# Kernel tuning notes

Hardware: AMD Instinct MI355X
Metric: run time of the kernel (lower is better)

Reference implementation:

```python
import jax, jax.numpy as jnp
import numpy as np

NODE_DIM = 128
NUM_IRREPS = 224          # 128 + 64 + 32 gates (one per irrep channel)
SPH_DIM = 480             # 128*1 + 64*3 + 32*5
HIDDEN = NODE_DIM + 2 * NUM_IRREPS  # 576
NUM_BASIS = 20
N_NODES = 10000
N_EDGES = 160000
# Each gate scalar is broadcast over its irrep's (2l+1) components.
_REPEATS = np.array([1] * 128 + [3] * 64 + [5] * 32)


def _expand_gate(g):
    # [E, 224] -> [E, 480], repeating each gate over its irrep dimension
    return jnp.repeat(g, _REPEATS, axis=-1, total_repeat_length=SPH_DIM)


def setup_inputs() -> dict:
    key = jax.random.key(0)
    ks = jax.random.split(key, 12)
    x_scalar = jax.random.normal(ks[0], (N_NODES, NODE_DIM), dtype=jnp.float32)
    x_spherical = jax.random.normal(ks[1], (N_NODES, SPH_DIM), dtype=jnp.float32)
    rbf = jax.random.uniform(ks[2], (N_EDGES, NUM_BASIS), dtype=jnp.float32)
    fcut = jax.random.uniform(ks[3], (N_EDGES, 1), dtype=jnp.float32)
    rsh = jax.random.normal(ks[4], (N_EDGES, SPH_DIM), dtype=jnp.float32)
    edge_index = jax.random.randint(ks[5], (2, N_EDGES), 0, N_NODES, dtype=jnp.int64)
    s1 = 1.0 / np.sqrt(NODE_DIM)
    s2 = 1.0 / np.sqrt(NUM_BASIS)
    W1 = jax.random.uniform(ks[6], (NODE_DIM, NODE_DIM), jnp.float32, -s1, s1)
    b1 = jnp.zeros((NODE_DIM,), jnp.float32)
    W2 = jax.random.uniform(ks[7], (NODE_DIM, HIDDEN), jnp.float32, -s1, s1)
    b2 = jnp.zeros((HIDDEN,), jnp.float32)
    Wr = jax.random.uniform(ks[8], (NUM_BASIS, HIDDEN), jnp.float32, -s2, s2)
    br = jnp.zeros((HIDDEN,), jnp.float32)
    return {"x_scalar": x_scalar, "x_spherical": x_spherical, "rbf": rbf,
            "fcut": fcut, "rsh": rsh, "edge_index": edge_index,
            "W1": W1, "b1": b1, "W2": W2, "b2": b2, "Wr": Wr, "br": br}


def reference(x_scalar, x_spherical, rbf, fcut, rsh, edge_index,
              W1, b1, W2, b2, Wr, br):
    src, dst = edge_index[0], edge_index[1]
    # scalar MLP: Linear -> SiLU -> Linear
    scalar_out = jax.nn.silu(x_scalar @ W1 + b1) @ W2 + b2          # [N, 576]
    filter_weight = (rbf @ Wr + br) * fcut                          # [E, 576]
    filter_out = scalar_out[dst] * filter_weight                    # [E, 576]
    gate_state = filter_out[:, :NUM_IRREPS]                         # [E, 224]
    gate_edge = filter_out[:, NUM_IRREPS:2 * NUM_IRREPS]            # [E, 224]
    message_scalar = filter_out[:, 2 * NUM_IRREPS:]                 # [E, 128]
    # ElementwiseTensorProduct(edge_irreps, '224x0e'): per-channel scalar gating
    message_spherical = (x_spherical[dst] * _expand_gate(gate_state)
                         + rsh * _expand_gate(gate_edge))           # [E, 480]
    new_scalar = x_scalar.at[src].add(message_scalar)
    new_spherical = x_spherical.at[src].add(message_spherical)
    return (new_scalar, new_spherical)
```

## Files before the change

kernel.cpp:

```cpp
#include <hip/hip_runtime.h>

#define NODE_DIM 128
#define NUM_IRREPS 224
#define SPH_DIM 480
#define HIDDEN 576
#define NUM_BASIS 20
#define N_NODES 10000
#define N_EDGES 160000
#define NPB 8

__global__ void init_out(const float* __restrict__ xs,
                         const float* __restrict__ xsp,
                         float* __restrict__ out,
                         int* __restrict__ counts) {
    const int stride = gridDim.x * blockDim.x;
    const int t0 = blockIdx.x * blockDim.x + threadIdx.x;
    for (int i = t0; i < N_NODES * NODE_DIM; i += stride) out[i] = xs[i];
    float* o2 = out + (size_t)N_NODES * NODE_DIM;
    for (int i = t0; i < N_NODES * SPH_DIM; i += stride) o2[i] = xsp[i];
    for (int i = t0; i < N_NODES; i += stride) counts[i] = 0;
}

__global__ __launch_bounds__(128) void node_mlp(
    const float* __restrict__ x,
    const float* __restrict__ W1, const float* __restrict__ b1,
    const float* __restrict__ W2, const float* __restrict__ b2,
    float* __restrict__ so) {
    __shared__ float xs[NPB][NODE_DIM];
    __shared__ float hs[NPB][NODE_DIM];
    const int tid = threadIdx.x;
    const int n0 = blockIdx.x * NPB;

    #pragma unroll
    for (int n = 0; n < NPB; ++n) {
        int node = n0 + n;
        xs[n][tid] = (node < N_NODES) ? x[(size_t)node * NODE_DIM + tid] : 0.f;
    }
    __syncthreads();

    float acc[NPB];
    #pragma unroll
    for (int n = 0; n < NPB; ++n) acc[n] = b1[tid];
    for (int k = 0; k < NODE_DIM; ++k) {
        float w = W1[k * NODE_DIM + tid];
        #pragma unroll
        for (int n = 0; n < NPB; ++n) acc[n] = fmaf(xs[n][k], w, acc[n]);
    }
    #pragma unroll
    for (int n = 0; n < NPB; ++n) {
        float v = acc[n];
        hs[n][tid] = v / (1.f + __expf(-v));
    }
    __syncthreads();

    for (int j = tid; j < HIDDEN; j += 128) {
        float a2[NPB];
        #pragma unroll
        for (int n = 0; n < NPB; ++n) a2[n] = b2[j];
        for (int k = 0; k < NODE_DIM; ++k) {
            float w = W2[k * HIDDEN + j];
            #pragma unroll
            for (int n = 0; n < NPB; ++n) a2[n] = fmaf(hs[n][k], w, a2[n]);
        }
        #pragma unroll
        for (int n = 0; n < NPB; ++n) {
            int node = n0 + n;
            if (node < N_NODES) so[(size_t)node * HIDDEN + j] = a2[n];
        }
    }
}

__global__ __launch_bounds__(256) void hist_kernel(const int* __restrict__ eidx,
                                                   int* __restrict__ counts) {
    int i = blockIdx.x * blockDim.x + threadIdx.x;
    if (i < N_EDGES) atomicAdd(&counts[eidx[i]], 1);
}

__global__ __launch_bounds__(1024) void scan_kernel(const int* __restrict__ counts,
                                                    int* __restrict__ offsets,
                                                    int* __restrict__ cursor) {
    __shared__ int wsum[16];
    const int tid = threadIdx.x;
    int vals[10];
    int run = 0;
    #pragma unroll
    for (int i = 0; i < 10; ++i) {
        int idx = tid * 10 + i;
        int c = (idx < N_NODES) ? counts[idx] : 0;
        vals[i] = run;
        run += c;
    }
    const int lane = tid & 63, w = tid >> 6;
    int inc = run;
    #pragma unroll
    for (int off = 1; off < 64; off <<= 1) {
        int v = __shfl_up(inc, off);
        if (lane >= off) inc += v;
    }
    if (lane == 63) wsum[w] = inc;
    __syncthreads();
    if (w == 0) {
        int v = (lane < 16) ? wsum[lane] : 0;
        #pragma unroll
        for (int off = 1; off < 16; off <<= 1) {
            int u = __shfl_up(v, off);
            if (lane >= off) v += u;
        }
        if (lane < 16) wsum[lane] = v;
    }
    __syncthreads();
    const int wbase = (w > 0) ? wsum[w - 1] : 0;
    const int base = wbase + inc - run;
    #pragma unroll
    for (int i = 0; i < 10; ++i) {
        int idx = tid * 10 + i;
        if (idx < N_NODES) {
            int v = base + vals[i];
            offsets[idx] = v;
            cursor[idx] = v;
        }
    }
    if (tid == 1023) offsets[N_NODES] = wbase + inc;
}

__global__ __launch_bounds__(256) void scatter_kernel(const int* __restrict__ eidx,
                                                      int* __restrict__ cursor,
                                                      int* __restrict__ edge_order) {
    int i = blockIdx.x * blockDim.x + threadIdx.x;
    if (i < N_EDGES) {
        int s = eidx[i];
        int pos = atomicAdd(&cursor[s], 1);
        edge_order[pos] = i;
    }
}

#define DOT20(a, WREG) do { \
    a = fmaf(q0.x, WREG[0], a);  a = fmaf(q0.y, WREG[1], a);  a = fmaf(q0.z, WREG[2], a);  a = fmaf(q0.w, WREG[3], a); \
    a = fmaf(q1.x, WREG[4], a);  a = fmaf(q1.y, WREG[5], a);  a = fmaf(q1.z, WREG[6], a);  a = fmaf(q1.w, WREG[7], a); \
    a = fmaf(q2.x, WREG[8], a);  a = fmaf(q2.y, WREG[9], a);  a = fmaf(q2.z, WREG[10], a); a = fmaf(q2.w, WREG[11], a); \
    a = fmaf(q3.x, WREG[12], a); a = fmaf(q3.y, WREG[13], a); a = fmaf(q3.z, WREG[14], a); a = fmaf(q3.w, WREG[15], a); \
    a = fmaf(q4.x, WREG[16], a); a = fmaf(q4.y, WREG[17], a); a = fmaf(q4.z, WREG[18], a); a = fmaf(q4.w, WREG[19], a); \
} while (0)

#define LOAD_PAYLOAD() do { \
    const float4* rq = (const float4*)(rbf + (size_t)eC * NUM_BASIS); \
    q0 = rq[0]; q1 = rq[1]; q2 = rq[2]; q3 = rq[3]; q4 = rq[4]; \
    const float* sod = so + (size_t)dC * HIDDEN; \
    s0 = sod[j0]; s1 = sod[j1]; \
    if (has2) s2 = sod[j2]; \
    const float* xd = xsp + (size_t)dC * SPH_DIM + d0; \
    const float* rd = rsh + (size_t)eC * SPH_DIM + d0; \
    x0 = xd[0]; r0 = rd[0]; \
    if (nd > 1) { x1 = xd[1]; r1 = rd[1]; } \
    if (nd > 2) { x2 = xd[2]; r2 = rd[2]; } \
} while (0)

__global__ __launch_bounds__(256, 4) void node_gather(
    const float* __restrict__ xsp,
    const float* __restrict__ rbf, const float* __restrict__ fcut,
    const float* __restrict__ rsh, const int* __restrict__ eidx,
    const float* __restrict__ Wr, const float* __restrict__ br,
    const float* __restrict__ so,
    const int* __restrict__ offsets, const int* __restrict__ edge_order,
    float* __restrict__ out_scalar, float* __restrict__ out_sph)
{
    const int t = threadIdx.x;
    const int n = blockIdx.x;
    const bool dup  = (t >= 224);
    const int  r    = dup ? (t - 32) : t;
    const int  j0   = r;
    const int  j1   = NUM_IRREPS + r;
    const bool has2 = (t < 128);
    const int  j2   = 2 * NUM_IRREPS + (t & 127);

    int nd, d0;
    if (t < 128)      { nd = 1; d0 = t; }
    else if (t < 192) { nd = 3; d0 = 128 + (t - 128) * 3; }
    else if (t < 224) { nd = 3; d0 = 320 + (t - 192) * 5; }
    else              { nd = 2; d0 = 320 + (t - 224) * 5 + 3; }

    float wr0[NUM_BASIS], wr1[NUM_BASIS], wr2[NUM_BASIS];
    #pragma unroll
    for (int k = 0; k < NUM_BASIS; ++k) {
        wr0[k] = Wr[k * HIDDEN + j0];
        wr1[k] = Wr[k * HIDDEN + j1];
        wr2[k] = has2 ? Wr[k * HIDDEN + j2] : 0.f;
    }
    const float br0 = br[j0], br1 = br[j1], br2 = has2 ? br[j2] : 0.f;

    const int beg  = offsets[n];
    const int end_ = offsets[n + 1];

    float accS = 0.f, accD0 = 0.f, accD1 = 0.f, accD2 = 0.f;

    if (beg < end_) {
        const int last = end_ - 1;
        const int i1 = min(beg + 1, last);
        const int i2 = min(beg + 2, last);
        const int i3 = min(beg + 3, last);
        int   eC = edge_order[beg];
        int   e1 = edge_order[i1];
        int   e2 = edge_order[i2];
        int   e3 = edge_order[i3];
        int   dC = eidx[N_EDGES + eC]; float fC = fcut[eC];
        int   d1 = eidx[N_EDGES + e1]; float f1 = fcut[e1];
        int   d2 = eidx[N_EDGES + e2]; float f2 = fcut[e2];

        float4 q0, q1, q2, q3, q4;
        float  s0, s1, s2 = 0.f, x0, x1 = 0.f, x2 = 0.f, r0, r1 = 0.f, r2 = 0.f;
        LOAD_PAYLOAD();

        for (int idx = beg; idx <= last; ++idx) {
            float a0 = br0, a1 = br1, a2 = br2;
            DOT20(a0, wr0);
            DOT20(a1, wr1);
            if (has2) { DOT20(a2, wr2); }
            const float fo0 = a0 * fC * s0;
            const float fo1 = a1 * fC * s1;
            if (has2) accS = fmaf(a2 * fC, s2, accS);
            accD0 = fmaf(x0, fo0, fmaf(r0, fo1, accD0));
            if (nd > 1) accD1 = fmaf(x1, fo0, fmaf(r1, fo1, accD1));
            if (nd > 2) accD2 = fmaf(x2, fo0, fmaf(r2, fo1, accD2));

            eC = e1; dC = d1; fC = f1;
            e1 = e2; d1 = d2; f1 = f2;
            LOAD_PAYLOAD();
            e2 = e3;
            d2 = eidx[N_EDGES + e3]; f2 = fcut[e3];
            e3 = edge_order[min(idx + 4, last)];
        }
    }

    if (t < 128) out_scalar[(size_t)n * NODE_DIM + t] += accS;
    float* od = out_sph + (size_t)n * SPH_DIM + d0;
    od[0] += accD0;
    if (nd > 1) od[1] += accD1;
    if (nd > 2) od[2] += accD2;
}

extern "C" void kernel_launch(void* const* d_in, const int* in_sizes, int n_in,
                              void* d_out, int out_size, void* d_ws, size_t ws_size,
                              hipStream_t stream) {
    const float* x_scalar    = (const float*)d_in[0];
    const float* x_spherical = (const float*)d_in[1];
    const float* rbf         = (const float*)d_in[2];
    const float* fcut        = (const float*)d_in[3];
    const float* rsh         = (const float*)d_in[4];
    const int*   eidx        = (const int*)d_in[5];
    const float* W1          = (const float*)d_in[6];
    const float* b1          = (const float*)d_in[7];
    const float* W2          = (const float*)d_in[8];
    const float* b2          = (const float*)d_in[9];
    const float* Wr          = (const float*)d_in[10];
    const float* br          = (const float*)d_in[11];

    float* out        = (float*)d_out;
    float* out_scalar = out;
    float* out_sph    = out + (size_t)N_NODES * NODE_DIM;

    float* scalar_out = (float*)d_ws;
    int*   counts     = (int*)(scalar_out + (size_t)N_NODES * HIDDEN);
    int*   offsets    = counts + N_NODES;
    int*   cursor     = offsets + N_NODES + 1;
    int*   edge_order = cursor + N_NODES;

    init_out<<<2048, 256, 0, stream>>>(x_scalar, x_spherical, out, counts);
    hist_kernel<<<(N_EDGES + 255) / 256, 256, 0, stream>>>(eidx, counts);
    scan_kernel<<<1, 1024, 0, stream>>>(counts, offsets, cursor);
    scatter_kernel<<<(N_EDGES + 255) / 256, 256, 0, stream>>>(eidx, cursor, edge_order);
    node_mlp<<<(N_NODES + NPB - 1) / NPB, 128, 0, stream>>>(x_scalar, W1, b1, W2, b2, scalar_out);
    node_gather<<<N_NODES, 256, 0, stream>>>(x_spherical, rbf, fcut, rsh, eidx,
                                             Wr, br, scalar_out, offsets, edge_order,
                                             out_scalar, out_sph);
}
```

Before: 335.5 us.

## Rebalance gather threads to 320 and double-buffer edge payload loads

The node gather kernel now uses 320 threads per block. The first 256 threads handle the spherical output and 64 extra threads each handle two scalar message channels, so no thread computes a third 20-wide dot product. The edge loop is unrolled by two with ping-pong payload registers, index prefetch runs deeper, and empty asm statements pin the Wr weights in VGPRs. The node MLP nodes-per-block also drops from 8 to 4. In exchange, per-thread register use goes up and each block carries an extra wavefront.

```diff
diff --git a/kernel.cpp b/kernel.cpp
--- a/kernel.cpp
+++ b/kernel.cpp
@@ -7,7 +7,7 @@
 #define NUM_BASIS 20
 #define N_NODES 10000
 #define N_EDGES 160000
-#define NPB 8
+#define NPB 4
 
 __global__ void init_out(const float* __restrict__ xs,
                          const float* __restrict__ xsp,
@@ -134,28 +134,51 @@
     }
 }
 
-#define DOT20(a, WREG) do { \
-    a = fmaf(q0.x, WREG[0], a);  a = fmaf(q0.y, WREG[1], a);  a = fmaf(q0.z, WREG[2], a);  a = fmaf(q0.w, WREG[3], a); \
-    a = fmaf(q1.x, WREG[4], a);  a = fmaf(q1.y, WREG[5], a);  a = fmaf(q1.z, WREG[6], a);  a = fmaf(q1.w, WREG[7], a); \
-    a = fmaf(q2.x, WREG[8], a);  a = fmaf(q2.y, WREG[9], a);  a = fmaf(q2.z, WREG[10], a); a = fmaf(q2.w, WREG[11], a); \
-    a = fmaf(q3.x, WREG[12], a); a = fmaf(q3.y, WREG[13], a); a = fmaf(q3.z, WREG[14], a); a = fmaf(q3.w, WREG[15], a); \
-    a = fmaf(q4.x, WREG[16], a); a = fmaf(q4.y, WREG[17], a); a = fmaf(q4.z, WREG[18], a); a = fmaf(q4.w, WREG[19], a); \
+#define PIN20(W) asm volatile("" : \
+ "+v"(W[0]),"+v"(W[1]),"+v"(W[2]),"+v"(W[3]),"+v"(W[4]), \
+ "+v"(W[5]),"+v"(W[6]),"+v"(W[7]),"+v"(W[8]),"+v"(W[9]), \
+ "+v"(W[10]),"+v"(W[11]),"+v"(W[12]),"+v"(W[13]),"+v"(W[14]), \
+ "+v"(W[15]),"+v"(W[16]),"+v"(W[17]),"+v"(W[18]),"+v"(W[19]))
+
+#define DOT20(a, W, Q0,Q1,Q2,Q3,Q4) do { \
+    a = fmaf(Q0.x, W[0], a);  a = fmaf(Q0.y, W[1], a);  a = fmaf(Q0.z, W[2], a);  a = fmaf(Q0.w, W[3], a); \
+    a = fmaf(Q1.x, W[4], a);  a = fmaf(Q1.y, W[5], a);  a = fmaf(Q1.z, W[6], a);  a = fmaf(Q1.w, W[7], a); \
+    a = fmaf(Q2.x, W[8], a);  a = fmaf(Q2.y, W[9], a);  a = fmaf(Q2.z, W[10], a); a = fmaf(Q2.w, W[11], a); \
+    a = fmaf(Q3.x, W[12], a); a = fmaf(Q3.y, W[13], a); a = fmaf(Q3.z, W[14], a); a = fmaf(Q3.w, W[15], a); \
+    a = fmaf(Q4.x, W[16], a); a = fmaf(Q4.y, W[17], a); a = fmaf(Q4.z, W[18], a); a = fmaf(Q4.w, W[19], a); \
 } while (0)
 
-#define LOAD_PAYLOAD() do { \
-    const float4* rq = (const float4*)(rbf + (size_t)eC * NUM_BASIS); \
-    q0 = rq[0]; q1 = rq[1]; q2 = rq[2]; q3 = rq[3]; q4 = rq[4]; \
-    const float* sod = so + (size_t)dC * HIDDEN; \
-    s0 = sod[j0]; s1 = sod[j1]; \
-    if (has2) s2 = sod[j2]; \
-    const float* xd = xsp + (size_t)dC * SPH_DIM + d0; \
-    const float* rd = rsh + (size_t)eC * SPH_DIM + d0; \
-    x0 = xd[0]; r0 = rd[0]; \
-    if (nd > 1) { x1 = xd[1]; r1 = rd[1]; } \
-    if (nd > 2) { x2 = xd[2]; r2 = rd[2]; } \
+#define LOADP(Q0,Q1,Q2,Q3,Q4, S0,S1, X0,X1,X2, R0,R1,R2, E, D) do { \
+    const float4* rq = (const float4*)(rbf + (size_t)(E) * NUM_BASIS); \
+    Q0 = rq[0]; Q1 = rq[1]; Q2 = rq[2]; Q3 = rq[3]; Q4 = rq[4]; \
+    const float* sod = so + (size_t)(D) * HIDDEN; \
+    S0 = sod[c0]; S1 = sod[c1]; \
+    if (sphMode) { \
+        const float* xd = xsp + (size_t)(D) * SPH_DIM + db; \
+        const float* rd = rsh + (size_t)(E) * SPH_DIM + db; \
+        X0 = xd[0]; R0 = rd[0]; \
+        if (nd > 1) { X1 = xd[1]; R1 = rd[1]; } \
+        if (nd > 2) { X2 = xd[2]; R2 = rd[2]; } \
+    } \
 } while (0)
 
-__global__ __launch_bounds__(256, 4) void node_gather(
+#define COMPUTE(Q0,Q1,Q2,Q3,Q4, S0,S1, X0,X1,X2, R0,R1,R2, FC) do { \
+    float a0 = bc0, a1 = bc1; \
+    DOT20(a0, w0, Q0,Q1,Q2,Q3,Q4); \
+    DOT20(a1, w1, Q0,Q1,Q2,Q3,Q4); \
+    if (sphMode) { \
+        const float fo0 = a0 * (FC) * S0; \
+        const float fo1 = a1 * (FC) * S1; \
+        accD0 = fmaf(X0, fo0, fmaf(R0, fo1, accD0)); \
+        if (nd > 1) accD1 = fmaf(X1, fo0, fmaf(R1, fo1, accD1)); \
+        if (nd > 2) accD2 = fmaf(X2, fo0, fmaf(R2, fo1, accD2)); \
+    } else { \
+        accA = fmaf(a0 * (FC), S0, accA); \
+        accB = fmaf(a1 * (FC), S1, accB); \
+    } \
+} while (0)
+
+__global__ __launch_bounds__(320, 3) void node_gather(
     const float* __restrict__ xsp,
     const float* __restrict__ rbf, const float* __restrict__ fcut,
     const float* __restrict__ rsh, const int* __restrict__ eidx,
@@ -166,76 +189,80 @@
 {
     const int t = threadIdx.x;
     const int n = blockIdx.x;
-    const bool dup  = (t >= 224);
-    const int  r    = dup ? (t - 32) : t;
-    const int  j0   = r;
-    const int  j1   = NUM_IRREPS + r;
-    const bool has2 = (t < 128);
-    const int  j2   = 2 * NUM_IRREPS + (t & 127);
-
-    int nd, d0;
-    if (t < 128)      { nd = 1; d0 = t; }
-    else if (t < 192) { nd = 3; d0 = 128 + (t - 128) * 3; }
-    else if (t < 224) { nd = 3; d0 = 320 + (t - 192) * 5; }
-    else              { nd = 2; d0 = 320 + (t - 224) * 5 + 3; }
-
-    float wr0[NUM_BASIS], wr1[NUM_BASIS], wr2[NUM_BASIS];
+    const bool sphMode = (t < 256);
+
+    int c0, c1;
+    if (t < 224)      { c0 = t;                  c1 = NUM_IRREPS + t; }
+    else if (t < 256) { c0 = t - 32;             c1 = NUM_IRREPS + (t - 32); }
+    else              { c0 = 448 + 2 * (t - 256); c1 = c0 + 1; }
+
+    int nd, db;
+    if (t < 128)      { nd = 1; db = t; }
+    else if (t < 192) { nd = 3; db = 128 + (t - 128) * 3; }
+    else if (t < 224) { nd = 3; db = 320 + (t - 192) * 5; }
+    else if (t < 256) { nd = 2; db = 320 + (t - 224) * 5 + 3; }
+    else              { nd = 0; db = 0; }
+
+    float w0[NUM_BASIS], w1[NUM_BASIS];
     #pragma unroll
     for (int k = 0; k < NUM_BASIS; ++k) {
-        wr0[k] = Wr[k * HIDDEN + j0];
-        wr1[k] = Wr[k * HIDDEN + j1];
-        wr2[k] = has2 ? Wr[k * HIDDEN + j2] : 0.f;
-    }
-    const float br0 = br[j0], br1 = br[j1], br2 = has2 ? br[j2] : 0.f;
+        w0[k] = Wr[k * HIDDEN + c0];
+        w1[k] = Wr[k * HIDDEN + c1];
+    }
+    const float bc0 = br[c0], bc1 = br[c1];
 
     const int beg  = offsets[n];
     const int end_ = offsets[n + 1];
 
-    float accS = 0.f, accD0 = 0.f, accD1 = 0.f, accD2 = 0.f;
+    float accD0 = 0.f, accD1 = 0.f, accD2 = 0.f, accA = 0.f, accB = 0.f;
 
     if (beg < end_) {
         const int last = end_ - 1;
-        const int i1 = min(beg + 1, last);
-        const int i2 = min(beg + 2, last);
-        const int i3 = min(beg + 3, last);
-        int   eC = edge_order[beg];
-        int   e1 = edge_order[i1];
-        int   e2 = edge_order[i2];
-        int   e3 = edge_order[i3];
-        int   dC = eidx[N_EDGES + eC]; float fC = fcut[eC];
-        int   d1 = eidx[N_EDGES + e1]; float f1 = fcut[e1];
-        int   d2 = eidx[N_EDGES + e2]; float f2 = fcut[e2];
-
-        float4 q0, q1, q2, q3, q4;
-        float  s0, s1, s2 = 0.f, x0, x1 = 0.f, x2 = 0.f, r0, r1 = 0.f, r2 = 0.f;
-        LOAD_PAYLOAD();
-
-        for (int idx = beg; idx <= last; ++idx) {
-            float a0 = br0, a1 = br1, a2 = br2;
-            DOT20(a0, wr0);
-            DOT20(a1, wr1);
-            if (has2) { DOT20(a2, wr2); }
-            const float fo0 = a0 * fC * s0;
-            const float fo1 = a1 * fC * s1;
-            if (has2) accS = fmaf(a2 * fC, s2, accS);
-            accD0 = fmaf(x0, fo0, fmaf(r0, fo1, accD0));
-            if (nd > 1) accD1 = fmaf(x1, fo0, fmaf(r1, fo1, accD1));
-            if (nd > 2) accD2 = fmaf(x2, fo0, fmaf(r2, fo1, accD2));
-
-            eC = e1; dC = d1; fC = f1;
-            e1 = e2; d1 = d2; f1 = f2;
-            LOAD_PAYLOAD();
-            e2 = e3;
-            d2 = eidx[N_EDGES + e3]; f2 = fcut[e3];
-            e3 = edge_order[min(idx + 4, last)];
-        }
-    }
-
-    if (t < 128) out_scalar[(size_t)n * NODE_DIM + t] += accS;
-    float* od = out_sph + (size_t)n * SPH_DIM + d0;
-    od[0] += accD0;
-    if (nd > 1) od[1] += accD1;
-    if (nd > 2) od[2] += accD2;
+        int e0 = edge_order[beg];
+        int e1 = edge_order[min(beg + 1, last)];
+        int e2 = edge_order[min(beg + 2, last)];
+        int e3 = edge_order[min(beg + 3, last)];
+        int e4 = edge_order[min(beg + 4, last)];
+        int e5 = edge_order[min(beg + 5, last)];
+        int d0q = eidx[N_EDGES + e0]; float f0 = fcut[e0];
+        int d1q = eidx[N_EDGES + e1]; float f1 = fcut[e1];
+        int d2q = eidx[N_EDGES + e2]; float f2 = fcut[e2];
+        int d3q = eidx[N_EDGES + e3]; float f3 = fcut[e3];
+
+        float4 qA0, qA1, qA2, qA3, qA4, qB0, qB1, qB2, qB3, qB4;
+        float sA0, sA1, xA0 = 0.f, xA1 = 0.f, xA2 = 0.f, rA0 = 0.f, rA1 = 0.f, rA2 = 0.f;
+        float sB0, sB1, xB0 = 0.f, xB1 = 0.f, xB2 = 0.f, rB0 = 0.f, rB1 = 0.f, rB2 = 0.f;
+        LOADP(qA0,qA1,qA2,qA3,qA4, sA0,sA1, xA0,xA1,xA2, rA0,rA1,rA2, e0, d0q);
+        LOADP(qB0,qB1,qB2,qB3,qB4, sB0,sB1, xB0,xB1,xB2, rB0,rB1,rB2, e1, d1q);
+
+        for (int idx = beg; idx <= last; idx += 2) {
+            PIN20(w0); PIN20(w1);
+            COMPUTE(qA0,qA1,qA2,qA3,qA4, sA0,sA1, xA0,xA1,xA2, rA0,rA1,rA2, f0);
+            LOADP(qA0,qA1,qA2,qA3,qA4, sA0,sA1, xA0,xA1,xA2, rA0,rA1,rA2, e2, d2q);
+            int   nd4 = eidx[N_EDGES + e4]; float nf4 = fcut[e4];
+            int   ne6 = edge_order[min(idx + 6, last)];
+            if (idx + 1 <= last) {
+                COMPUTE(qB0,qB1,qB2,qB3,qB4, sB0,sB1, xB0,xB1,xB2, rB0,rB1,rB2, f1);
+            }
+            LOADP(qB0,qB1,qB2,qB3,qB4, sB0,sB1, xB0,xB1,xB2, rB0,rB1,rB2, e3, d3q);
+            int   nd5 = eidx[N_EDGES + e5]; float nf5 = fcut[e5];
+            int   ne7 = edge_order[min(idx + 7, last)];
+            e0 = e2; e1 = e3; e2 = e4; e3 = e5; e4 = ne6; e5 = ne7;
+            d0q = d2q; d1q = d3q; d2q = nd4; d3q = nd5;
+            f0 = f2; f1 = f3; f2 = nf4; f3 = nf5;
+        }
+    }
+
+    if (sphMode) {
+        float* od = out_sph + (size_t)n * SPH_DIM + db;
+        od[0] += accD0;
+        if (nd > 1) od[1] += accD1;
+        if (nd > 2) od[2] += accD2;
+    } else {
+        float* osr = out_scalar + (size_t)n * NODE_DIM + 2 * (t - 256);
+        osr[0] += accA;
+        osr[1] += accB;
+    }
 }
 
 extern "C" void kernel_launch(void* const* d_in, const int* in_sizes, int n_in,
@@ -269,7 +296,7 @@
     scan_kernel<<<1, 1024, 0, stream>>>(counts, offsets, cursor);
     scatter_kernel<<<(N_EDGES + 255) / 256, 256, 0, stream>>>(eidx, cursor, edge_order);
     node_mlp<<<(N_NODES + NPB - 1) / NPB, 128, 0, stream>>>(x_scalar, W1, b1, W2, b2, scalar_out);
-    node_gather<<<N_NODES, 256, 0, stream>>>(x_spherical, rbf, fcut, rsh, eidx,
+    node_gather<<<N_NODES, 320, 0, stream>>>(x_spherical, rbf, fcut, rsh, eidx,
                                              Wr, br, scalar_out, offsets, edge_order,
                                              out_scalar, out_sph);
 }
```

New measurement: 308.8 us. -7.9%, faster.

## Coalesce gather via shared-memory gate exchange and fuse output init into gather

Applied to the files above, without the earlier changes.

Restructures node_gather so each thread computes one irrep-channel gate pair, stores it in a double-buffered shared array, and reads coalesced x_spherical and rsh elements (t and 256+t) whose gates it looks up from shared memory. This replaces the strided per-thread component loads of the old mapping. The init_out copy kernel is removed: the gather writes x plus the accumulated message directly, so only the counts need zeroing. A software pipeline with explicit lgkmcnt waits and barriers overlaps the next edge's loads with the current compute, at the cost of one block barrier per edge and more registers from dropping the occupancy hint.

```diff
diff --git a/kernel.cpp b/kernel.cpp
--- a/kernel.cpp
+++ b/kernel.cpp
@@ -9,16 +9,9 @@
 #define N_EDGES 160000
 #define NPB 8
 
-__global__ void init_out(const float* __restrict__ xs,
-                         const float* __restrict__ xsp,
-                         float* __restrict__ out,
-                         int* __restrict__ counts) {
-    const int stride = gridDim.x * blockDim.x;
-    const int t0 = blockIdx.x * blockDim.x + threadIdx.x;
-    for (int i = t0; i < N_NODES * NODE_DIM; i += stride) out[i] = xs[i];
-    float* o2 = out + (size_t)N_NODES * NODE_DIM;
-    for (int i = t0; i < N_NODES * SPH_DIM; i += stride) o2[i] = xsp[i];
-    for (int i = t0; i < N_NODES; i += stride) counts[i] = 0;
+__global__ void init_counts(int* __restrict__ counts) {
+    int i = blockIdx.x * blockDim.x + threadIdx.x;
+    if (i < N_NODES) counts[i] = 0;
 }
 
 __global__ __launch_bounds__(128) void node_mlp(
@@ -134,28 +127,45 @@
     }
 }
 
-#define DOT20(a, WREG) do { \
-    a = fmaf(q0.x, WREG[0], a);  a = fmaf(q0.y, WREG[1], a);  a = fmaf(q0.z, WREG[2], a);  a = fmaf(q0.w, WREG[3], a); \
-    a = fmaf(q1.x, WREG[4], a);  a = fmaf(q1.y, WREG[5], a);  a = fmaf(q1.z, WREG[6], a);  a = fmaf(q1.w, WREG[7], a); \
-    a = fmaf(q2.x, WREG[8], a);  a = fmaf(q2.y, WREG[9], a);  a = fmaf(q2.z, WREG[10], a); a = fmaf(q2.w, WREG[11], a); \
-    a = fmaf(q3.x, WREG[12], a); a = fmaf(q3.y, WREG[13], a); a = fmaf(q3.z, WREG[14], a); a = fmaf(q3.w, WREG[15], a); \
-    a = fmaf(q4.x, WREG[16], a); a = fmaf(q4.y, WREG[17], a); a = fmaf(q4.z, WREG[18], a); a = fmaf(q4.w, WREG[19], a); \
+#define DOTN(a, W) do { \
+    a = fmaf(qn0.x, W[0], a);  a = fmaf(qn0.y, W[1], a);  a = fmaf(qn0.z, W[2], a);  a = fmaf(qn0.w, W[3], a); \
+    a = fmaf(qn1.x, W[4], a);  a = fmaf(qn1.y, W[5], a);  a = fmaf(qn1.z, W[6], a);  a = fmaf(qn1.w, W[7], a); \
+    a = fmaf(qn2.x, W[8], a);  a = fmaf(qn2.y, W[9], a);  a = fmaf(qn2.z, W[10], a); a = fmaf(qn2.w, W[11], a); \
+    a = fmaf(qn3.x, W[12], a); a = fmaf(qn3.y, W[13], a); a = fmaf(qn3.z, W[14], a); a = fmaf(qn3.w, W[15], a); \
+    a = fmaf(qn4.x, W[16], a); a = fmaf(qn4.y, W[17], a); a = fmaf(qn4.z, W[18], a); a = fmaf(qn4.w, W[19], a); \
 } while (0)
 
-#define LOAD_PAYLOAD() do { \
-    const float4* rq = (const float4*)(rbf + (size_t)eC * NUM_BASIS); \
-    q0 = rq[0]; q1 = rq[1]; q2 = rq[2]; q3 = rq[3]; q4 = rq[4]; \
-    const float* sod = so + (size_t)dC * HIDDEN; \
-    s0 = sod[j0]; s1 = sod[j1]; \
-    if (has2) s2 = sod[j2]; \
-    const float* xd = xsp + (size_t)dC * SPH_DIM + d0; \
-    const float* rd = rsh + (size_t)eC * SPH_DIM + d0; \
-    x0 = xd[0]; r0 = rd[0]; \
-    if (nd > 1) { x1 = xd[1]; r1 = rd[1]; } \
-    if (nd > 2) { x2 = xd[2]; r2 = rd[2]; } \
+#define LOADN(E, D, F) do { \
+    const float4* rq_ = (const float4*)(rbf + (size_t)(E) * NUM_BASIS); \
+    qn0 = rq_[0]; qn1 = rq_[1]; qn2 = rq_[2]; qn3 = rq_[3]; qn4 = rq_[4]; \
+    const float* sod_ = so + (size_t)(D) * HIDDEN; \
+    s0n = sod_[c0]; s1n = sod_[c1]; s2n = hasSc ? sod_[c2] : 0.f; \
+    const float* x_ = xsp + (size_t)(D) * SPH_DIM; \
+    const float* r_ = rsh + (size_t)(E) * SPH_DIM; \
+    x1n = x_[t]; r1n = r_[t]; \
+    if (t < 224) { x2n = x_[256 + t]; r2n = r_[256 + t]; } \
+    fn = (F); \
 } while (0)
 
-__global__ __launch_bounds__(256, 4) void node_gather(
+#define LOADW(E, D, F) do { \
+    const float4* rq_ = (const float4*)(rbf + (size_t)(E) * NUM_BASIS); \
+    qw0 = rq_[0]; qw1 = rq_[1]; qw2 = rq_[2]; qw3 = rq_[3]; qw4 = rq_[4]; \
+    const float* sod_ = so + (size_t)(D) * HIDDEN; \
+    s0w = sod_[c0]; s1w = sod_[c1]; s2w = hasSc ? sod_[c2] : 0.f; \
+    const float* x_ = xsp + (size_t)(D) * SPH_DIM; \
+    const float* r_ = rsh + (size_t)(E) * SPH_DIM; \
+    x1w = x_[t]; r1w = r_[t]; \
+    if (t < 224) { x2w = x_[256 + t]; r2w = r_[256 + t]; } \
+    fw = (F); \
+} while (0)
+
+#define LGKM_BARRIER() do { \
+    asm volatile("s_waitcnt lgkmcnt(0)" ::: "memory"); \
+    __builtin_amdgcn_s_barrier(); \
+} while (0)
+
+__global__ __launch_bounds__(256) void node_gather(
+    const float* __restrict__ xscal,
     const float* __restrict__ xsp,
     const float* __restrict__ rbf, const float* __restrict__ fcut,
     const float* __restrict__ rsh, const int* __restrict__ eidx,
@@ -164,78 +174,105 @@
     const int* __restrict__ offsets, const int* __restrict__ edge_order,
     float* __restrict__ out_scalar, float* __restrict__ out_sph)
 {
+    __shared__ float2 fo_s[2][NUM_IRREPS];
     const int t = threadIdx.x;
     const int n = blockIdx.x;
-    const bool dup  = (t >= 224);
-    const int  r    = dup ? (t - 32) : t;
-    const int  j0   = r;
-    const int  j1   = NUM_IRREPS + r;
-    const bool has2 = (t < 128);
-    const int  j2   = 2 * NUM_IRREPS + (t & 127);
-
-    int nd, d0;
-    if (t < 128)      { nd = 1; d0 = t; }
-    else if (t < 192) { nd = 3; d0 = 128 + (t - 128) * 3; }
-    else if (t < 224) { nd = 3; d0 = 320 + (t - 192) * 5; }
-    else              { nd = 2; d0 = 320 + (t - 224) * 5 + 3; }
-
-    float wr0[NUM_BASIS], wr1[NUM_BASIS], wr2[NUM_BASIS];
+    const bool hasIr = (t < 224);
+    const bool hasSc = (t < 128);
+    const int c0 = t;
+    const int c1 = NUM_IRREPS + t;
+    const int c2 = 2 * NUM_IRREPS + t;
+
+    const int g1i = (t < 128) ? t : (128 + (t - 128) / 3);
+    const int g2i = (t < 64) ? (128 + (128 + t) / 3) : (192 + (t - 64) / 5);
+
+    float w0[NUM_BASIS], w1[NUM_BASIS], w2[NUM_BASIS];
     #pragma unroll
     for (int k = 0; k < NUM_BASIS; ++k) {
-        wr0[k] = Wr[k * HIDDEN + j0];
-        wr1[k] = Wr[k * HIDDEN + j1];
-        wr2[k] = has2 ? Wr[k * HIDDEN + j2] : 0.f;
-    }
-    const float br0 = br[j0], br1 = br[j1], br2 = has2 ? br[j2] : 0.f;
+        w0[k] = hasIr ? Wr[k * HIDDEN + c0] : 0.f;
+        w1[k] = hasIr ? Wr[k * HIDDEN + c1] : 0.f;
+        w2[k] = hasSc ? Wr[k * HIDDEN + c2] : 0.f;
+    }
+    const float bc0 = hasIr ? br[c0] : 0.f;
+    const float bc1 = hasIr ? br[c1] : 0.f;
+    const float bc2 = hasSc ? br[c2] : 0.f;
 
     const int beg  = offsets[n];
     const int end_ = offsets[n + 1];
 
-    float accS = 0.f, accD0 = 0.f, accD1 = 0.f, accD2 = 0.f;
+    float accS = 0.f, accD1 = 0.f, accD2 = 0.f;
 
     if (beg < end_) {
         const int last = end_ - 1;
-        const int i1 = min(beg + 1, last);
-        const int i2 = min(beg + 2, last);
-        const int i3 = min(beg + 3, last);
-        int   eC = edge_order[beg];
-        int   e1 = edge_order[i1];
-        int   e2 = edge_order[i2];
-        int   e3 = edge_order[i3];
-        int   dC = eidx[N_EDGES + eC]; float fC = fcut[eC];
-        int   d1 = eidx[N_EDGES + e1]; float f1 = fcut[e1];
-        int   d2 = eidx[N_EDGES + e2]; float f2 = fcut[e2];
-
-        float4 q0, q1, q2, q3, q4;
-        float  s0, s1, s2 = 0.f, x0, x1 = 0.f, x2 = 0.f, r0, r1 = 0.f, r2 = 0.f;
-        LOAD_PAYLOAD();
-
-        for (int idx = beg; idx <= last; ++idx) {
-            float a0 = br0, a1 = br1, a2 = br2;
-            DOT20(a0, wr0);
-            DOT20(a1, wr1);
-            if (has2) { DOT20(a2, wr2); }
-            const float fo0 = a0 * fC * s0;
-            const float fo1 = a1 * fC * s1;
-            if (has2) accS = fmaf(a2 * fC, s2, accS);
-            accD0 = fmaf(x0, fo0, fmaf(r0, fo1, accD0));
-            if (nd > 1) accD1 = fmaf(x1, fo0, fmaf(r1, fo1, accD1));
-            if (nd > 2) accD2 = fmaf(x2, fo0, fmaf(r2, fo1, accD2));
-
-            eC = e1; dC = d1; fC = f1;
-            e1 = e2; d1 = d2; f1 = f2;
-            LOAD_PAYLOAD();
-            e2 = e3;
-            d2 = eidx[N_EDGES + e3]; f2 = fcut[e3];
-            e3 = edge_order[min(idx + 4, last)];
-        }
-    }
-
-    if (t < 128) out_scalar[(size_t)n * NODE_DIM + t] += accS;
-    float* od = out_sph + (size_t)n * SPH_DIM + d0;
-    od[0] += accD0;
-    if (nd > 1) od[1] += accD1;
-    if (nd > 2) od[2] += accD2;
+        int p = 0;
+
+        float4 qn0, qn1, qn2, qn3, qn4, qw0, qw1, qw2, qw3, qw4;
+        float s0n, s1n, s2n, s0w, s1w, s2w;
+        float x1n, x2n = 0.f, r1n, r2n = 0.f;
+        float x1w, x2w = 0.f, r1w, r2w = 0.f;
+        float x1c, x2c = 0.f, r1c, r2c = 0.f;
+        float fn, fw;
+
+        {
+            int eA = edge_order[beg];
+            int dA = eidx[N_EDGES + eA];
+            float fA = fcut[eA];
+            LOADN(eA, dA, fA);
+        }
+        {
+            float a0 = bc0, a1 = bc1, a2 = bc2;
+            DOTN(a0, w0); DOTN(a1, w1);
+            if (hasSc) DOTN(a2, w2);
+            if (hasIr) fo_s[0][t] = make_float2(a0 * fn * s0n, a1 * fn * s1n);
+            if (hasSc) accS = fmaf(a2 * fn, s2n, accS);
+        }
+        x1c = x1n; r1c = r1n; x2c = x2n; r2c = r2n;
+        {
+            int eB = edge_order[min(beg + 1, last)];
+            int dB = eidx[N_EDGES + eB];
+            float fB = fcut[eB];
+            LOADN(eB, dB, fB);
+        }
+        int e2m = edge_order[min(beg + 2, last)];
+        int d2m = eidx[N_EDGES + e2m];
+        float f2m = fcut[e2m];
+        int e3m = edge_order[min(beg + 3, last)];
+
+        LGKM_BARRIER();
+
+        for (int idx = beg; idx < end_; ++idx) {
+            LOADW(e2m, d2m, f2m);
+            {
+                float a0 = bc0, a1 = bc1, a2 = bc2;
+                DOTN(a0, w0); DOTN(a1, w1);
+                if (hasSc) DOTN(a2, w2);
+                if (hasIr) fo_s[p ^ 1][t] = make_float2(a0 * fn * s0n, a1 * fn * s1n);
+                if (hasSc && (idx + 1 < end_)) accS = fmaf(a2 * fn, s2n, accS);
+            }
+            {
+                float2 fa = fo_s[p][g1i];
+                accD1 = fmaf(x1c, fa.x, fmaf(r1c, fa.y, accD1));
+                if (t < 224) {
+                    float2 fb = fo_s[p][g2i];
+                    accD2 = fmaf(x2c, fb.x, fmaf(r2c, fb.y, accD2));
+                }
+            }
+            LGKM_BARRIER();
+            x1c = x1n; r1c = r1n; x2c = x2n; r2c = r2n;
+            qn0 = qw0; qn1 = qw1; qn2 = qw2; qn3 = qw3; qn4 = qw4;
+            s0n = s0w; s1n = s1w; s2n = s2w; fn = fw;
+            x1n = x1w; r1n = r1w; x2n = x2w; r2n = r2w;
+            e2m = e3m;
+            d2m = eidx[N_EDGES + e3m];
+            f2m = fcut[e3m];
+            e3m = edge_order[min(idx + 4, last)];
+            p ^= 1;
+        }
+    }
+
+    if (t < 128) out_scalar[(size_t)n * NODE_DIM + t] = xscal[(size_t)n * NODE_DIM + t] + accS;
+    out_sph[(size_t)n * SPH_DIM + t] = xsp[(size_t)n * SPH_DIM + t] + accD1;
+    if (t < 224) out_sph[(size_t)n * SPH_DIM + 256 + t] = xsp[(size_t)n * SPH_DIM + 256 + t] + accD2;
 }
 
 extern "C" void kernel_launch(void* const* d_in, const int* in_sizes, int n_in,
@@ -264,12 +301,12 @@
     int*   cursor     = offsets + N_NODES + 1;
     int*   edge_order = cursor + N_NODES;
 
-    init_out<<<2048, 256, 0, stream>>>(x_scalar, x_spherical, out, counts);
+    init_counts<<<(N_NODES + 255) / 256, 256, 0, stream>>>(counts);
     hist_kernel<<<(N_EDGES + 255) / 256, 256, 0, stream>>>(eidx, counts);
     scan_kernel<<<1, 1024, 0, stream>>>(counts, offsets, cursor);
     scatter_kernel<<<(N_EDGES + 255) / 256, 256, 0, stream>>>(eidx, cursor, edge_order);
     node_mlp<<<(N_NODES + NPB - 1) / NPB, 128, 0, stream>>>(x_scalar, W1, b1, W2, b2, scalar_out);
-    node_gather<<<N_NODES, 256, 0, stream>>>(x_spherical, rbf, fcut, rsh, eidx,
+    node_gather<<<N_NODES, 256, 0, stream>>>(x_scalar, x_spherical, rbf, fcut, rsh, eidx,
                                              Wr, br, scalar_out, offsets, edge_order,
                                              out_scalar, out_sph);
 }
```

Result: slower. 351.0 us (+4.6%).
